# Performance work log

Hardware: AMD Instinct MI355X
Metric: run time of the kernel (lower is better)

The kernel has to match this reference:

```python
import jax, jax.numpy as jnp
import numpy as np

S = 256          # image_size
NEAR = 0.1       # NMR default near plane
FAR = 100.0      # NMR default far plane / background depth
CHUNK = 16       # faces per scan step (memory control)
EYE_Z = -1.0 / np.tan(np.radians(30.0))  # camera_mode='look', viewing_angle=30


def _render(verts, faces):
    """Orthographic rasterizer matching NMR forward: silhouette + depth.

    verts: [B,N,3] float, faces: [F,3] int (shared across batch).
    """
    B = verts.shape[0]
    # NMR forward flips the y axis, then the 'look' camera (default direction
    # [0,0,1], up [0,1,0]) reduces to a translation by -eye.
    v = verts * jnp.array([1.0, -1.0, 1.0], verts.dtype)
    v = v - jnp.array([0.0, 0.0, EYE_Z], verts.dtype)

    F = faces.shape[0]
    pad = (-F) % CHUNK
    # padded faces are (0,0,0) -> zero-area triangles, rejected by the area test
    faces_p = jnp.concatenate([faces, jnp.zeros((pad, 3), faces.dtype)], 0)
    nch = faces_p.shape[0] // CHUNK
    fv = v[:, faces_p]                                  # [B, Fp, 3, 3]
    fv = jnp.moveaxis(fv.reshape(B, nch, CHUNK, 3, 3), 1, 0)  # [nch, B, C, 3, 3]

    # NMR pixel-center convention: x_p = (2*xi + 1 - S)/S, row 0 at +y (top)
    xs = (2.0 * jnp.arange(S, dtype=verts.dtype) + 1.0 - S) / S
    px = xs[None, None, None, :]          # [1,1,1,W]
    py = (-xs)[None, None, :, None]       # [1,1,H,1]

    def body(zbuf, fvc):                  # fvc: [B, C, 3, 3]
        x, y, z = fvc[..., 0], fvc[..., 1], fvc[..., 2]
        x0, x1, x2 = x[..., 0], x[..., 1], x[..., 2]
        y0, y1, y2 = y[..., 0], y[..., 1], y[..., 2]
        z0, z1, z2 = z[..., 0], z[..., 1], z[..., 2]
        # signed area*2; dividing edge functions by it handles both windings
        area = (x1 - x0) * (y2 - y0) - (x2 - x0) * (y1 - y0)      # [B,C]
        ok = jnp.abs(area) > 1e-7
        inv_area = jnp.where(ok, 1.0 / jnp.where(ok, area, 1.0), 0.0)[..., None, None]

        def edge(xa, ya, xb, yb):
            # signed area of (p, a, b), expanded as linear function of (px,py)
            a = xa * yb - xb * ya
            b = ya - yb
            c = xb - xa
            return a[..., None, None] + b[..., None, None] * px + c[..., None, None] * py

        w0 = edge(x1, y1, x2, y2) * inv_area        # [B,C,H,W]
        w1 = edge(x2, y2, x0, y0) * inv_area
        w2 = 1.0 - w0 - w1
        inside = (w0 >= 0) & (w1 >= 0) & (w2 >= 0) & ok[..., None, None]
        # perspective-correct depth interpolation as in NMR's rasterizer
        zinv = (w0 / z0[..., None, None] + w1 / z1[..., None, None]
                + w2 / z2[..., None, None])
        zq = 1.0 / jnp.maximum(zinv, 1e-8)
        cand = jnp.where(inside & (zq > NEAR) & (zq < FAR), zq, FAR)
        return jnp.minimum(zbuf, cand.min(axis=1)), None

    zbuf0 = jnp.full((B, S, S), FAR, verts.dtype)
    zbuf, _ = jax.lax.scan(body, zbuf0, fv)
    sil = (zbuf < FAR).astype(verts.dtype)
    return sil, zbuf


def setup_inputs() -> dict:
    key = jax.random.key(0)
    k1, k2, k3 = jax.random.split(key, 3)
    B, N, F = 16, 778, 1538
    xy = jax.random.uniform(k1, (B, N, 2), minval=-0.8, maxval=0.8)
    z = jax.random.uniform(k2, (B, N, 1), minval=-0.5, maxval=0.8)
    verts = jnp.concatenate([xy, z], axis=-1).astype(jnp.float32)
    faces = jax.random.randint(k3, (F, 3), 0, N, dtype=jnp.int32)
    return {"verts": verts, "faces": faces}


def reference(verts, faces):
    # returns (silhouettes [B,H,W], depth [B,H,W]) like NMR.forward(depth=True)
    return _render(verts, faces)
```

## Files before the change

kernel.cpp:

```cpp
#include <hip/hip_runtime.h>
#include <hip/hip_fp16.h>
#include <stdint.h>

#define SS 256
#define FAR_F 100.0f
#define REG 32
#define NREG 64
#define NCH 3
#define CAPP 448
#define CAPQ 352
#define CAPFQ 224
#define OVN  96
#define DEFN 32

struct __align__(16) PackedCoef {
    float4 q0;
    float4 q1;
    float4 q2;
};

__global__ void nmr_prep(const float* __restrict__ verts,
                         const int* __restrict__ faces,
                         PackedCoef* __restrict__ pc,
                         uint32_t* __restrict__ bbx,
                         int B, int N, int F)
{
#pragma clang fp contract(off)
    int idx = blockIdx.x * blockDim.x + threadIdx.x;
    if (idx >= B * F) return;
    int b = idx / F;
    int f = idx - b * F;

    int i0 = faces[3 * f + 0], i1 = faces[3 * f + 1], i2 = faces[3 * f + 2];
    const float* vb = verts + (size_t)(3 * N) * b;
    const float EZ = -1.7320508075688772f;

    float x0 = vb[3 * i0 + 0], y0 = -vb[3 * i0 + 1], z0 = vb[3 * i0 + 2] - EZ;
    float x1 = vb[3 * i1 + 0], y1 = -vb[3 * i1 + 1], z1 = vb[3 * i1 + 2] - EZ;
    float x2 = vb[3 * i2 + 0], y2 = -vb[3 * i2 + 1], z2 = vb[3 * i2 + 2] - EZ;

    float area = (x1 - x0) * (y2 - y0) - (x2 - x0) * (y1 - y0);
    bool ok = fabsf(area) > 1e-7f;
    float ia = ok ? (1.0f / area) : 0.0f;

    float A0 = (x1 * y2 - x2 * y1) * ia, B0 = (y1 - y2) * ia, C0 = (x2 - x1) * ia;
    float A1 = (x2 * y0 - x0 * y2) * ia, B1 = (y2 - y0) * ia, C1 = (x0 - x2) * ia;
    float rz0 = 1.0f / z0, rz1 = 1.0f / z1, rz2 = 1.0f / z2;
    float d0 = rz0 - rz2, d1 = rz1 - rz2;
    float Z0 = rz2 + A0 * d0 + A1 * d1;
    float Zx = B0 * d0 + B1 * d1;
    float Zy = C0 * d0 + C1 * d1;
    float S = fabsf(A0) + fabsf(B0) + fabsf(C0) + fabsf(A1) + fabsf(B1) + fabsf(C1) + 1.0f;
    float ef = 3e-6f * S;

    uint32_t bb = 255u | (0u << 8) | (255u << 16) | (0u << 24);
    if (ok) {
        float xmn = fminf(x0, fminf(x1, x2)), xmx = fmaxf(x0, fmaxf(x1, x2));
        float ymn = fminf(y0, fminf(y1, y2)), ymx = fmaxf(y0, fmaxf(y1, y2));
        int jlo = (int)floorf(128.0f * (xmn + 1.0f) - 0.5f) - 1;
        int jhi = (int)ceilf (128.0f * (xmx + 1.0f) - 0.5f) + 1;
        int ilo = (int)floorf((255.0f - 256.0f * ymx) * 0.5f) - 1;
        int ihi = (int)ceilf ((255.0f - 256.0f * ymn) * 0.5f) + 1;
        jlo = max(0, min(255, jlo)); jhi = max(0, min(255, jhi));
        ilo = max(0, min(255, ilo)); ihi = max(0, min(255, ihi));
        if (jhi >= jlo && ihi >= ilo)
            bb = (uint32_t)jlo | ((uint32_t)jhi << 8) | ((uint32_t)ilo << 16) | ((uint32_t)ihi << 24);
    }

    PackedCoef c;
    c.q0 = make_float4(A0, B0, C0, A1);
    c.q1 = make_float4(B1, C1, Zx, Zy);
    c.q2 = make_float4(Z0, ef, __uint_as_float(bb), __uint_as_float((uint32_t)f));
    pc[idx] = c;
    bbx[idx] = bb;
}

__device__ __forceinline__ void exact_body(
    float Zx, float Zy, float Z0, int fid,
    float px, float py0, float py1, float py2, float py3,
    const float* __restrict__ verts, const int* __restrict__ faces, int N, int b,
    float& best0, float& best1, float& best2, float& best3)
{
#pragma clang fp contract(off)
    float zbv = __builtin_fmaf(Zx, px, Z0);
    float zi0 = __builtin_fmaf(Zy, py0, zbv);
    float zi1 = __builtin_fmaf(Zy, py1, zbv);
    float zi2 = __builtin_fmaf(Zy, py2, zbv);
    float zi3 = __builtin_fmaf(Zy, py3, zbv);
    fid = __builtin_amdgcn_readfirstlane(fid);
    int i0f = faces[3 * fid + 0], i1f = faces[3 * fid + 1], i2f = faces[3 * fid + 2];
    const float* vb = verts + (size_t)(3 * N) * b;
    float x0 = vb[3 * i0f + 0], y0 = -vb[3 * i0f + 1];
    float x1 = vb[3 * i1f + 0], y1 = -vb[3 * i1f + 1];
    float x2 = vb[3 * i2f + 0], y2 = -vb[3 * i2f + 1];
    float area = (x1 - x0) * (y2 - y0) - (x2 - x0) * (y1 - y0);
    float ia = 1.0f / area;
    float a0 = x1 * y2 - x2 * y1, b0e = y1 - y2, c0e = x2 - x1;
    float a1 = x2 * y0 - x0 * y2, b1e = y2 - y0, c1e = x0 - x2;
    float e0b = a0 + b0e * px;
    float e1b = a1 + b1e * px;
    { float u0 = (e0b + c0e * py0) * ia, u1 = (e1b + c1e * py0) * ia;
      if (fminf(u0, fminf(u1, (1.0f - u0) - u1)) >= 0.0f) best0 = fmaxf(best0, zi0); }
    { float u0 = (e0b + c0e * py1) * ia, u1 = (e1b + c1e * py1) * ia;
      if (fminf(u0, fminf(u1, (1.0f - u0) - u1)) >= 0.0f) best1 = fmaxf(best1, zi1); }
    { float u0 = (e0b + c0e * py2) * ia, u1 = (e1b + c1e * py2) * ia;
      if (fminf(u0, fminf(u1, (1.0f - u0) - u1)) >= 0.0f) best2 = fmaxf(best2, zi2); }
    { float u0 = (e0b + c0e * py3) * ia, u1 = (e1b + c1e * py3) * ia;
      if (fminf(u0, fminf(u1, (1.0f - u0) - u1)) >= 0.0f) best3 = fmaxf(best3, zi3); }
}

__device__ __forceinline__ void face_body(
    float4 q0, float4 q1, float4 q2,
    float px, float py0, float py1, float py2, float py3,
    const float* __restrict__ verts, const int* __restrict__ faces, int N, int b,
    float& best0, float& best1, float& best2, float& best3)
{
#pragma clang fp contract(off)
    const float ef = q2.y;
    float w0b = __builtin_fmaf(q0.y, px, q0.x);
    float w1b = __builtin_fmaf(q1.x, px, q0.w);
    float zbv = __builtin_fmaf(q1.z, px, q2.x);
    float w0_0 = __builtin_fmaf(q0.z, py0, w0b), w1_0 = __builtin_fmaf(q1.y, py0, w1b);
    float w0_1 = __builtin_fmaf(q0.z, py1, w0b), w1_1 = __builtin_fmaf(q1.y, py1, w1b);
    float w0_2 = __builtin_fmaf(q0.z, py2, w0b), w1_2 = __builtin_fmaf(q1.y, py2, w1b);
    float w0_3 = __builtin_fmaf(q0.z, py3, w0b), w1_3 = __builtin_fmaf(q1.y, py3, w1b);
    float m0 = fminf(w0_0, fminf(w1_0, (1.0f - w0_0) - w1_0));
    float m1 = fminf(w0_1, fminf(w1_1, (1.0f - w0_1) - w1_1));
    float m2 = fminf(w0_2, fminf(w1_2, (1.0f - w0_2) - w1_2));
    float m3 = fminf(w0_3, fminf(w1_3, (1.0f - w0_3) - w1_3));
    float zi0 = __builtin_fmaf(q1.w, py0, zbv);
    float zi1 = __builtin_fmaf(q1.w, py1, zbv);
    float zi2 = __builtin_fmaf(q1.w, py2, zbv);
    float zi3 = __builtin_fmaf(q1.w, py3, zbv);
    bool amb = (fabsf(m0) <= ef) | (fabsf(m1) <= ef) | (fabsf(m2) <= ef) | (fabsf(m3) <= ef);
    if (__any(amb)) {
        exact_body(q1.z, q1.w, q2.x, (int)__float_as_uint(q2.w),
                   px, py0, py1, py2, py3, verts, faces, N, b, best0, best1, best2, best3);
        return;
    }
    best0 = (m0 > ef) ? fmaxf(best0, zi0) : best0;
    best1 = (m1 > ef) ? fmaxf(best1, zi1) : best1;
    best2 = (m2 > ef) ? fmaxf(best2, zi2) : best2;
    best3 = (m3 > ef) ? fmaxf(best3, zi3) : best3;
}

__device__ __forceinline__ float wave_min_f(float x) {
    #pragma unroll
    for (int m = 1; m < 64; m <<= 1) x = fminf(x, __shfl_xor(x, m));
    return x;
}

__global__ __launch_bounds__(256, 4) void nmr_raster(
    const PackedCoef* __restrict__ pc,
    const uint32_t* __restrict__ bbx,
    const float* __restrict__ verts,
    const int* __restrict__ faces,
    uint32_t* __restrict__ zu,
    int B, int N, int F, int CH)
{
#pragma clang fp contract(off)
    __shared__ float4   pool[2 * CAPP];
    __shared__ uint2    zef[CAPP];
    __shared__ float4   qfull[4][CAPFQ];
    __shared__ __align__(16) uint32_t qpart[4][CAPQ];
    __shared__ uint16_t ovl[OVN];
    __shared__ uint16_t dlist[4][DEFN];
    __shared__ int qcnt[4], qfcnt[4], cnt_p, cnt_o;

    const int tid = threadIdx.x;
    const int bid = blockIdx.x;
    const int ch = bid % NCH; int t = bid / NCH;
    const int reg = t % NREG; const int b = t / NREG;
    const int rj0 = (reg & 7) * REG;
    const int ri0 = (reg >> 3) * REG;

    if (tid == 0) { cnt_p = 0; cnt_o = 0; }
    if (tid < 4) { qcnt[tid] = 0; qfcnt[tid] = 0; }
    __syncthreads();

    const int f0 = ch * CH, f1 = min(F, f0 + CH);
    const uint32_t* bb = bbx + (size_t)b * F;
    const PackedCoef* pb = pc + (size_t)b * F;

    const float cx0 = (float)(2 * rj0 + 1 - SS) * (1.0f / SS);
    const float cx1 = (float)(2 * (rj0 + 15) + 1 - SS) * (1.0f / SS);
    const float cx2 = (float)(2 * (rj0 + 16) + 1 - SS) * (1.0f / SS);
    const float cx3 = (float)(2 * (rj0 + 31) + 1 - SS) * (1.0f / SS);
    const float cy0 = (float)(SS - 1 - 2 * ri0) * (1.0f / SS);
    const float cy1 = (float)(SS - 1 - 2 * (ri0 + 15)) * (1.0f / SS);
    const float cy2 = (float)(SS - 1 - 2 * (ri0 + 16)) * (1.0f / SS);
    const float cy3 = (float)(SS - 1 - 2 * (ri0 + 31)) * (1.0f / SS);

    for (int f = f0 + tid; f < f1; f += 256) {
        uint32_t v = bb[f];
        int jlo = v & 255, jhi = (v >> 8) & 255, ilo = (v >> 16) & 255, ihi = (int)(v >> 24);
        if (jlo > rj0 + REG - 1 || jhi < rj0 || ilo > ri0 + REG - 1 || ihi < ri0) continue;
        PackedCoef P = pb[f];
        const float A0 = P.q0.x, B0 = P.q0.y, C0 = P.q0.z;
        const float A1 = P.q0.w, B1 = P.q1.x, C1 = P.q1.y;
        const float Zx = P.q1.z, Zy = P.q1.w, Z0 = P.q2.x, ef = P.q2.y;
        const float A2 = (1.0f - A0) - A1, B2 = (0.0f - B0) - B1, C2 = (0.0f - C0) - C1;
        const float Rm = 2.0f * ef;

        float bn[3][2], bX[3][2], tn[3][2], tX[3][2];
        {
            float e_b0, e_b1, e_b2, e_b3, e_t0, e_t1, e_t2, e_t3;
            e_b0 = __builtin_fmaf(B0, cx0, A0); e_b1 = __builtin_fmaf(B0, cx1, A0);
            e_b2 = __builtin_fmaf(B0, cx2, A0); e_b3 = __builtin_fmaf(B0, cx3, A0);
            e_t0 = C0 * cy0; e_t1 = C0 * cy1; e_t2 = C0 * cy2; e_t3 = C0 * cy3;
            bn[0][0] = fminf(e_b0, e_b1); bX[0][0] = fmaxf(e_b0, e_b1);
            bn[0][1] = fminf(e_b2, e_b3); bX[0][1] = fmaxf(e_b2, e_b3);
            tn[0][0] = fminf(e_t0, e_t1); tX[0][0] = fmaxf(e_t0, e_t1);
            tn[0][1] = fminf(e_t2, e_t3); tX[0][1] = fmaxf(e_t2, e_t3);
            e_b0 = __builtin_fmaf(B1, cx0, A1); e_b1 = __builtin_fmaf(B1, cx1, A1);
            e_b2 = __builtin_fmaf(B1, cx2, A1); e_b3 = __builtin_fmaf(B1, cx3, A1);
            e_t0 = C1 * cy0; e_t1 = C1 * cy1; e_t2 = C1 * cy2; e_t3 = C1 * cy3;
            bn[1][0] = fminf(e_b0, e_b1); bX[1][0] = fmaxf(e_b0, e_b1);
            bn[1][1] = fminf(e_b2, e_b3); bX[1][1] = fmaxf(e_b2, e_b3);
            tn[1][0] = fminf(e_t0, e_t1); tX[1][0] = fmaxf(e_t0, e_t1);
            tn[1][1] = fminf(e_t2, e_t3); tX[1][1] = fmaxf(e_t2, e_t3);
            e_b0 = __builtin_fmaf(B2, cx0, A2); e_b1 = __builtin_fmaf(B2, cx1, A2);
            e_b2 = __builtin_fmaf(B2, cx2, A2); e_b3 = __builtin_fmaf(B2, cx3, A2);
            e_t0 = C2 * cy0; e_t1 = C2 * cy1; e_t2 = C2 * cy2; e_t3 = C2 * cy3;
            bn[2][0] = fminf(e_b0, e_b1); bX[2][0] = fmaxf(e_b0, e_b1);
            bn[2][1] = fminf(e_b2, e_b3); bX[2][1] = fmaxf(e_b2, e_b3);
            tn[2][0] = fminf(e_t0, e_t1); tX[2][0] = fmaxf(e_t0, e_t1);
            tn[2][1] = fminf(e_t2, e_t3); tX[2][1] = fmaxf(e_t2, e_t3);
        }
        float zb0 = __builtin_fmaf(Zx, cx0, Z0), zb1 = __builtin_fmaf(Zx, cx1, Z0);
        float zb2 = __builtin_fmaf(Zx, cx2, Z0), zb3 = __builtin_fmaf(Zx, cx3, Z0);
        float zt0 = Zy * cy0, zt1 = Zy * cy1, zt2 = Zy * cy2, zt3 = Zy * cy3;
        float zbX0 = fmaxf(zb0, zb1), zbX1 = fmaxf(zb2, zb3);
        float ztX0 = fmaxf(zt0, zt1), ztX1 = fmaxf(zt2, zt3);

        int partMask = 0;
        float key0f = 0.0f, key1f = 0.0f, key2f = 0.0f, key3f = 0.0f;

        #pragma unroll
        for (int q = 0; q < 4; ++q) {
            const int qx = q & 1, qy = q >> 1;
            const int qj0 = rj0 + qx * 16, qi0 = ri0 + qy * 16;
            if (jlo > qj0 + 15 || jhi < qj0 || ilo > qi0 + 15 || ihi < qi0) continue;
            float e0x = bX[0][qx] + tX[0][qy];
            float e1x = bX[1][qx] + tX[1][qy];
            float e2x = bX[2][qx] + tX[2][qy];
            if (e0x < -Rm || e1x < -Rm || e2x < -Rm) continue;
            float km = (qx ? zbX1 : zbX0) + (qy ? ztX1 : ztX0);
            float key = fmaxf(km + __builtin_fmaf(fabsf(km), 1e-6f, 1e-5f), 0.0f);
            float e0n = bn[0][qx] + tn[0][qy];
            float e1n = bn[1][qx] + tn[1][qy];
            float e2n = bn[2][qx] + tn[2][qy];
            bool full = (e0n > Rm) && (e1n > Rm) && (e2n > Rm);
            if (full) {
                int s = atomicAdd(&qfcnt[q], 1);
                if (s < CAPFQ) { qfull[q][s] = make_float4(Z0, Zx, Zy, key); continue; }
            }
            partMask |= 1 << q;
            if (q == 0) key0f = key; else if (q == 1) key1f = key;
            else if (q == 2) key2f = key; else key3f = key;
        }

        if (partMask) {
            int p = atomicAdd(&cnt_p, 1);
            if (p < CAPP) {
                pool[2 * p + 0] = P.q0;
                pool[2 * p + 1] = P.q1;
                uint32_t efh = (uint32_t)__half_as_ushort(__float2half(ef * 1.002f));
                zef[p] = make_uint2(__float_as_uint(Z0), ((uint32_t)f << 16) | efh);
                #pragma unroll
                for (int q = 0; q < 4; ++q) {
                    if (!((partMask >> q) & 1)) continue;
                    float key = (q == 0) ? key0f : (q == 1) ? key1f : (q == 2) ? key2f : key3f;
                    uint32_t entry = ((__float_as_uint(key) + 0xFFFu) & 0xFFFFF000u) | (uint32_t)p;
                    int s = atomicAdd(&qcnt[q], 1);
                    if (s < CAPQ) qpart[q][s] = entry;
                    else { int o = atomicAdd(&cnt_o, 1); if (o < OVN) ovl[o] = (uint16_t)f; }
                }
            } else {
                int o = atomicAdd(&cnt_o, 1);
                if (o < OVN) ovl[o] = (uint16_t)f;
            }
        }
    }
    __syncthreads();

    const int no = min(cnt_o, OVN);
    #pragma unroll
    for (int q = 0; q < 4; ++q) {
        int n = min(qcnt[q], CAPQ); int n4 = (n + 3) & ~3;
        for (int i = n + tid; i < n4; i += 256) qpart[q][i] = 0u;
    }
    __syncthreads();

    const int lane = tid & 63, w = tid >> 6;
    const int wj0 = rj0 + ((w & 1) << 4);
    const int wi0 = ri0 + ((w >> 1) << 4);
    const int j = wj0 + (lane & 15);
    const int i0r = wi0 + (lane >> 4);
    const float px = (float)(2 * j + 1 - SS) * (1.0f / SS);
    const float py0 = (float)(SS - 1 - 2 * (i0r + 0))  * (1.0f / SS);
    const float py1 = (float)(SS - 1 - 2 * (i0r + 4))  * (1.0f / SS);
    const float py2 = (float)(SS - 1 - 2 * (i0r + 8))  * (1.0f / SS);
    const float py3 = (float)(SS - 1 - 2 * (i0r + 12)) * (1.0f / SS);

    float best0 = 0.0f, best1 = 0.0f, best2 = 0.0f, best3 = 0.0f;

    {
        const float4* qf = &qfull[w][0];
        const int nq = min(qfcnt[w], CAPFQ);
        float lm = 0.0f;
        for (int k = 0; k < nq; ++k) {
            if ((k & 15) == 0) lm = wave_min_f(fminf(fminf(best0, best1), fminf(best2, best3)));
            float4 z = qf[k];
            if (z.w <= lm) continue;
            float zb = __builtin_fmaf(z.y, px, z.x);
            best0 = fmaxf(best0, __builtin_fmaf(z.z, py0, zb));
            best1 = fmaxf(best1, __builtin_fmaf(z.z, py1, zb));
            best2 = fmaxf(best2, __builtin_fmaf(z.z, py2, zb));
            best3 = fmaxf(best3, __builtin_fmaf(z.z, py3, zb));
        }
    }

    int dcnt = 0;
    {
        const uint32_t* ql = &qpart[w][0];
        const int nq = min(qcnt[w], CAPQ);
        const int nq4 = (nq + 3) & ~3;
        for (int base = 0; base < nq4; base += 16) {
            float lm = wave_min_f(fminf(fminf(best0, best1), fminf(best2, best3)));
            uint32_t lmU = __float_as_uint(lm);
            int gend = min(base + 16, nq4);
            for (int g = base; g < gend; g += 4) {
                uint4 kk = *reinterpret_cast<const uint4*>(&ql[g]);
                uint32_t k0 = kk.x & 0xFFFFF000u, k1 = kk.y & 0xFFFFF000u;
                uint32_t k2 = kk.z & 0xFFFFF000u, k3 = kk.w & 0xFFFFF000u;
                uint32_t gmax = max(max(k0, k1), max(k2, k3));
                if (gmax <= lmU) continue;
                #pragma unroll
                for (int u = 0; u < 4; ++u) {
                    uint32_t e = (u == 0) ? kk.x : (u == 1) ? kk.y : (u == 2) ? kk.z : kk.w;
                    if ((e & 0xFFFFF000u) <= lmU) continue;
                    int k = (int)(e & 0xFFFu);
                    float4 q0 = pool[2 * k + 0];
                    float4 q1 = pool[2 * k + 1];
                    uint2  ze = zef[k];
                    float Z0 = __uint_as_float(ze.x);
                    float ef = __half2float(__ushort_as_half((unsigned short)(ze.y & 0xFFFFu)));
                    float w0b = __builtin_fmaf(q0.y, px, q0.x);
                    float w1b = __builtin_fmaf(q1.x, px, q0.w);
                    float zbv = __builtin_fmaf(q1.z, px, Z0);
                    float w0_0 = __builtin_fmaf(q0.z, py0, w0b), w1_0 = __builtin_fmaf(q1.y, py0, w1b);
                    float w0_1 = __builtin_fmaf(q0.z, py1, w0b), w1_1 = __builtin_fmaf(q1.y, py1, w1b);
                    float w0_2 = __builtin_fmaf(q0.z, py2, w0b), w1_2 = __builtin_fmaf(q1.y, py2, w1b);
                    float w0_3 = __builtin_fmaf(q0.z, py3, w0b), w1_3 = __builtin_fmaf(q1.y, py3, w1b);
                    float m0 = fminf(w0_0, fminf(w1_0, (1.0f - w0_0) - w1_0));
                    float m1 = fminf(w0_1, fminf(w1_1, (1.0f - w0_1) - w1_1));
                    float m2 = fminf(w0_2, fminf(w1_2, (1.0f - w0_2) - w1_2));
                    float m3 = fminf(w0_3, fminf(w1_3, (1.0f - w0_3) - w1_3));
                    float zi0 = __builtin_fmaf(q1.w, py0, zbv);
                    float zi1 = __builtin_fmaf(q1.w, py1, zbv);
                    float zi2 = __builtin_fmaf(q1.w, py2, zbv);
                    float zi3 = __builtin_fmaf(q1.w, py3, zbv);
                    best0 = (m0 > ef) ? fmaxf(best0, zi0) : best0;
                    best1 = (m1 > ef) ? fmaxf(best1, zi1) : best1;
                    best2 = (m2 > ef) ? fmaxf(best2, zi2) : best2;
                    best3 = (m3 > ef) ? fmaxf(best3, zi3) : best3;
                    float mabs = fminf(fminf(fabsf(m0), fabsf(m1)), fminf(fabsf(m2), fabsf(m3)));
                    if (__any(mabs <= ef)) {
                        if (dcnt == DEFN) {
                            for (int d = 0; d < dcnt; ++d) {
                                int kk2 = (int)dlist[w][d];
                                float4 p1 = pool[2 * kk2 + 1];
                                uint2  z2 = zef[kk2];
                                exact_body(p1.z, p1.w, __uint_as_float(z2.x), (int)(z2.y >> 16),
                                           px, py0, py1, py2, py3, verts, faces, N, b,
                                           best0, best1, best2, best3);
                            }
                            dcnt = 0;
                        }
                        if (lane == 0) dlist[w][dcnt] = (uint16_t)k;
                        dcnt++;
                    }
                }
            }
        }
    }
    for (int d = 0; d < dcnt; ++d) {
        int kk2 = (int)dlist[w][d];
        float4 p1 = pool[2 * kk2 + 1];
        uint2  z2 = zef[kk2];
        exact_body(p1.z, p1.w, __uint_as_float(z2.x), (int)(z2.y >> 16),
                   px, py0, py1, py2, py3, verts, faces, N, b,
                   best0, best1, best2, best3);
    }

    const PackedCoef* pb2 = pc + (size_t)b * F;
    for (int k = 0; k < no; ++k) {
        int fid = __builtin_amdgcn_readfirstlane((int)ovl[k]);
        float4 q2 = pb2[fid].q2;
        uint32_t bv = __float_as_uint(q2.z);
        int jlo = bv & 255, jhi = (bv >> 8) & 255, ilo = (bv >> 16) & 255, ihi = (int)(bv >> 24);
        if (jlo > wj0 + 15 || jhi < wj0 || ilo > wi0 + 15 || ihi < wi0) continue;
        face_body(pb2[fid].q0, pb2[fid].q1, q2,
                  px, py0, py1, py2, py3, verts, faces, N, b,
                  best0, best1, best2, best3);
    }

    const size_t obase = (size_t)b * (SS * SS) + (size_t)i0r * SS + j;
    if (best0 > 0.0f) atomicMin(&zu[obase + 0 * 4 * SS], __float_as_uint(1.0f / best0));
    if (best1 > 0.0f) atomicMin(&zu[obase + 1 * 4 * SS], __float_as_uint(1.0f / best1));
    if (best2 > 0.0f) atomicMin(&zu[obase + 2 * 4 * SS], __float_as_uint(1.0f / best2));
    if (best3 > 0.0f) atomicMin(&zu[obase + 3 * 4 * SS], __float_as_uint(1.0f / best3));
}

__global__ void nmr_final(float* __restrict__ out, int B)
{
    int idx = blockIdx.x * 256 + threadIdx.x;
    if (idx >= B * SS * SS) return;
    uint32_t* zu = (uint32_t*)(out + (size_t)B * SS * SS);
    uint32_t u = zu[idx];
    bool cov = (u != 0xFFFFFFFFu);
    out[idx] = cov ? 1.0f : 0.0f;
    ((float*)zu)[idx] = cov ? __uint_as_float(u) : FAR_F;
}

extern "C" void kernel_launch(void* const* d_in, const int* in_sizes, int n_in,
                              void* d_out, int out_size, void* d_ws, size_t ws_size,
                              hipStream_t stream)
{
    const float* verts = (const float*)d_in[0];
    const int*   faces = (const int*)d_in[1];
    float* out = (float*)d_out;

    const int B = out_size / (2 * SS * SS);
    const int F = in_sizes[1] / 3;
    const int N = in_sizes[0] / (3 * B);

    PackedCoef* pc = (PackedCoef*)d_ws;
    uint32_t*  bbx = (uint32_t*)((char*)d_ws + (size_t)B * F * sizeof(PackedCoef));
    uint32_t*  zu  = (uint32_t*)(out + (size_t)B * SS * SS);

    hipMemsetAsync(zu, 0xFF, (size_t)B * SS * SS * sizeof(uint32_t), stream);

    const int total = B * F;
    nmr_prep<<<(total + 255) / 256, 256, 0, stream>>>(verts, faces, pc, bbx, B, N, F);

    const int CH = (F + NCH - 1) / NCH;
    nmr_raster<<<B * NREG * NCH, 256, 0, stream>>>(pc, bbx, verts, faces, zu, B, N, F, CH);

    nmr_final<<<(B * SS * SS + 255) / 256, 256, 0, stream>>>(out, B);
}
```

Measured before the change: 78.01 us.

## Sort per-quadrant face lists by depth key to enable early loop exit

```diff
diff --git a/kernel.cpp b/kernel.cpp
--- a/kernel.cpp
+++ b/kernel.cpp
@@ -8,8 +8,8 @@
 #define NREG 64
 #define NCH 3
 #define CAPP 448
-#define CAPQ 352
-#define CAPFQ 224
+#define CAPQ 320
+#define CAPFQ 192
 #define OVN  96
 #define DEFN 32
 
@@ -150,6 +150,23 @@
     return x;
 }
 
+__device__ __forceinline__ uint32_t wave_sort64_desc(uint32_t e) {
+    const int lane = (int)(threadIdx.x & 63);
+    #pragma unroll
+    for (int k = 2; k <= 64; k <<= 1) {
+        #pragma unroll
+        for (int j = k >> 1; j > 0; j >>= 1) {
+            uint32_t other = __shfl_xor(e, j);
+            int partner = lane ^ j;
+            bool up = ((lane & k) != 0);
+            bool keepSmall = ((lane < partner) == up);
+            uint32_t mn = min(e, other), mx = max(e, other);
+            e = keepSmall ? mn : mx;
+        }
+    }
+    return e;
+}
+
 __global__ __launch_bounds__(256, 4) void nmr_raster(
     const PackedCoef* __restrict__ pc,
     const uint32_t* __restrict__ bbx,
@@ -162,6 +179,7 @@
     __shared__ float4   pool[2 * CAPP];
     __shared__ uint2    zef[CAPP];
     __shared__ float4   qfull[4][CAPFQ];
+    __shared__ __align__(16) uint32_t fkidx[4][CAPFQ];
     __shared__ __align__(16) uint32_t qpart[4][CAPQ];
     __shared__ uint16_t ovl[OVN];
     __shared__ uint16_t dlist[4][DEFN];
@@ -253,7 +271,11 @@
             bool full = (e0n > Rm) && (e1n > Rm) && (e2n > Rm);
             if (full) {
                 int s = atomicAdd(&qfcnt[q], 1);
-                if (s < CAPFQ) { qfull[q][s] = make_float4(Z0, Zx, Zy, key); continue; }
+                if (s < CAPFQ) {
+                    qfull[q][s] = make_float4(Z0, Zx, Zy, key);
+                    fkidx[q][s] = ((__float_as_uint(key) + 0xFFFu) & 0xFFFFF000u) | (uint32_t)s;
+                    continue;
+                }
             }
             partMask |= 1 << q;
             if (q == 0) key0f = key; else if (q == 1) key1f = key;
@@ -289,6 +311,8 @@
     for (int q = 0; q < 4; ++q) {
         int n = min(qcnt[q], CAPQ); int n4 = (n + 3) & ~3;
         for (int i = n + tid; i < n4; i += 256) qpart[q][i] = 0u;
+        int nf = min(qfcnt[q], CAPFQ); int nf4 = (nf + 3) & ~3;
+        for (int i = nf + tid; i < nf4; i += 256) fkidx[q][i] = 0u;
     }
     __syncthreads();
 
@@ -303,39 +327,67 @@
     const float py2 = (float)(SS - 1 - 2 * (i0r + 8))  * (1.0f / SS);
     const float py3 = (float)(SS - 1 - 2 * (i0r + 12)) * (1.0f / SS);
 
+    const int nq  = min(qcnt[w], CAPQ);  const int nq4 = (nq + 3) & ~3;
+    const int nfq = min(qfcnt[w], CAPFQ); const int nf4 = (nfq + 3) & ~3;
+    for (int wb = 0; wb < nq4; wb += 64) {
+        int ix = wb + lane;
+        uint32_t e = (ix < nq4) ? qpart[w][ix] : 0u;
+        e = wave_sort64_desc(e);
+        if (ix < nq4) qpart[w][ix] = e;
+    }
+    for (int wb = 0; wb < nf4; wb += 64) {
+        int ix = wb + lane;
+        uint32_t e = (ix < nf4) ? fkidx[w][ix] : 0u;
+        e = wave_sort64_desc(e);
+        if (ix < nf4) fkidx[w][ix] = e;
+    }
+
     float best0 = 0.0f, best1 = 0.0f, best2 = 0.0f, best3 = 0.0f;
 
     {
+        const uint32_t* fl = &fkidx[w][0];
         const float4* qf = &qfull[w][0];
-        const int nq = min(qfcnt[w], CAPFQ);
-        float lm = 0.0f;
-        for (int k = 0; k < nq; ++k) {
-            if ((k & 15) == 0) lm = wave_min_f(fminf(fminf(best0, best1), fminf(best2, best3)));
-            float4 z = qf[k];
-            if (z.w <= lm) continue;
-            float zb = __builtin_fmaf(z.y, px, z.x);
-            best0 = fmaxf(best0, __builtin_fmaf(z.z, py0, zb));
-            best1 = fmaxf(best1, __builtin_fmaf(z.z, py1, zb));
-            best2 = fmaxf(best2, __builtin_fmaf(z.z, py2, zb));
-            best3 = fmaxf(best3, __builtin_fmaf(z.z, py3, zb));
+        float lm = 0.0f; uint32_t lmU = 0u;
+        int cnt = 0;
+        for (int wb = 0; wb < nf4; wb += 64) {
+            int wend = min(wb + 64, nf4);
+            for (int g = wb; g < wend; g += 4) {
+                if ((cnt++ & 3) == 0) {
+                    lm = wave_min_f(fminf(fminf(best0, best1), fminf(best2, best3)));
+                    lmU = __float_as_uint(lm);
+                }
+                uint4 kk = *reinterpret_cast<const uint4*>(&fl[g]);
+                if ((kk.x & 0xFFFFF000u) <= lmU) break;
+                #pragma unroll
+                for (int u = 0; u < 4; ++u) {
+                    uint32_t e = (u == 0) ? kk.x : (u == 1) ? kk.y : (u == 2) ? kk.z : kk.w;
+                    if ((e & 0xFFFFF000u) <= lmU) continue;
+                    float4 z = qf[e & 0xFFFu];
+                    float zb = __builtin_fmaf(z.y, px, z.x);
+                    best0 = fmaxf(best0, __builtin_fmaf(z.z, py0, zb));
+                    best1 = fmaxf(best1, __builtin_fmaf(z.z, py1, zb));
+                    best2 = fmaxf(best2, __builtin_fmaf(z.z, py2, zb));
+                    best3 = fmaxf(best3, __builtin_fmaf(z.z, py3, zb));
+                }
+            }
         }
     }
 
     int dcnt = 0;
     {
         const uint32_t* ql = &qpart[w][0];
-        const int nq = min(qcnt[w], CAPQ);
-        const int nq4 = (nq + 3) & ~3;
-        for (int base = 0; base < nq4; base += 16) {
-            float lm = wave_min_f(fminf(fminf(best0, best1), fminf(best2, best3)));
-            uint32_t lmU = __float_as_uint(lm);
-            int gend = min(base + 16, nq4);
-            for (int g = base; g < gend; g += 4) {
+        float lm = wave_min_f(fminf(fminf(best0, best1), fminf(best2, best3)));
+        uint32_t lmU = __float_as_uint(lm);
+        int cnt = 0;
+        for (int wb = 0; wb < nq4; wb += 64) {
+            int wend = min(wb + 64, nq4);
+            for (int g = wb; g < wend; g += 4) {
+                if ((cnt++ & 3) == 0) {
+                    lm = wave_min_f(fminf(fminf(best0, best1), fminf(best2, best3)));
+                    lmU = __float_as_uint(lm);
+                }
                 uint4 kk = *reinterpret_cast<const uint4*>(&ql[g]);
-                uint32_t k0 = kk.x & 0xFFFFF000u, k1 = kk.y & 0xFFFFF000u;
-                uint32_t k2 = kk.z & 0xFFFFF000u, k3 = kk.w & 0xFFFFF000u;
-                uint32_t gmax = max(max(k0, k1), max(k2, k3));
-                if (gmax <= lmU) continue;
+                if ((kk.x & 0xFFFFF000u) <= lmU) break;
                 #pragma unroll
                 for (int u = 0; u < 4; ++u) {
                     uint32_t e = (u == 0) ? kk.x : (u == 1) ? kk.y : (u == 2) ? kk.z : kk.w;
```

Result: faster. 76.38 us (-2.1%).
